# Performance work log

Measured on AMD Instinct MI355X. Metric: run time of the kernel, lower is better.

Reference implementation:

```python
import jax, jax.numpy as jnp
import numpy as np

N_NODES = 50000
N_EDGES = 800000
IN_NF = 128
OUT_NF = 128
HID = 128
EDGE_NF = 16
N_LAYERS = 4
EPS = 1e-5


def _ln(x, g, b):
    mu = jnp.mean(x, axis=-1, keepdims=True)
    var = jnp.mean(jnp.square(x - mu), axis=-1, keepdims=True)
    return (x - mu) * jax.lax.rsqrt(var + EPS) * g + b


def setup_inputs() -> dict:
    key = jax.random.key(0)
    ks = iter(jax.random.split(key, 64))

    def lin(out_d, in_d):
        w = jax.random.normal(next(ks), (out_d, in_d), dtype=jnp.float32) * 0.02
        b = jnp.zeros((out_d,), dtype=jnp.float32)
        return w, b

    def stack(fn):
        outs = [fn() for _ in range(N_LAYERS)]
        return tuple(jnp.stack([o[i] for o in outs]) for i in range(len(outs[0])))

    h = jax.random.normal(next(ks), (N_NODES, IN_NF), dtype=jnp.float32)
    edges = jax.random.randint(next(ks), (2, N_EDGES), 0, N_NODES, dtype=jnp.int32)
    edge_attr = jax.random.normal(next(ks), (N_EDGES, EDGE_NF), dtype=jnp.float32)

    emb_in_w1, emb_in_b1 = lin(HID, IN_NF)
    emb_in_w2, emb_in_b2 = lin(HID, HID)
    emb_out_w1, emb_out_b1 = lin(HID, HID)
    emb_out_w2, emb_out_b2 = lin(OUT_NF, HID)

    norm_g, norm_b = stack(lambda: (jnp.ones((HID,), jnp.float32), jnp.zeros((HID,), jnp.float32)))
    edge_w1, edge_b1 = stack(lambda: lin(HID, 2 * HID + EDGE_NF))
    edge_ln_g, edge_ln_b = stack(lambda: (jnp.ones((HID,), jnp.float32), jnp.zeros((HID,), jnp.float32)))
    edge_w2, edge_b2 = stack(lambda: lin(HID, HID))
    node_w1, node_b1 = stack(lambda: lin(HID, 2 * HID))
    node_ln_g, node_ln_b = stack(lambda: (jnp.ones((HID,), jnp.float32), jnp.zeros((HID,), jnp.float32)))
    node_w2, node_b2 = stack(lambda: lin(HID, HID))

    return dict(h=h, edges=edges, edge_attr=edge_attr,
                emb_in_w1=emb_in_w1, emb_in_b1=emb_in_b1, emb_in_w2=emb_in_w2, emb_in_b2=emb_in_b2,
                norm_g=norm_g, norm_b=norm_b,
                edge_w1=edge_w1, edge_b1=edge_b1, edge_ln_g=edge_ln_g, edge_ln_b=edge_ln_b,
                edge_w2=edge_w2, edge_b2=edge_b2,
                node_w1=node_w1, node_b1=node_b1, node_ln_g=node_ln_g, node_ln_b=node_ln_b,
                node_w2=node_w2, node_b2=node_b2,
                emb_out_w1=emb_out_w1, emb_out_b1=emb_out_b1, emb_out_w2=emb_out_w2, emb_out_b2=emb_out_b2)


def _gnn(h, edges, edge_attr,
         emb_in_w1, emb_in_b1, emb_in_w2, emb_in_b2,
         norm_g, norm_b, edge_w1, edge_b1, edge_ln_g, edge_ln_b, edge_w2, edge_b2,
         node_w1, node_b1, node_ln_g, node_ln_b, node_w2, node_b2,
         emb_out_w1, emb_out_b1, emb_out_w2, emb_out_b2):
    row, col = edges[0], edges[1]
    n = h.shape[0]

    # embedding_in: Linear -> SiLU -> Linear
    h = jax.nn.silu(h @ emb_in_w1.T + emb_in_b1) @ emb_in_w2.T + emb_in_b2

    def layer(h, p):
        (ng, nb, ew1, eb1, elg, elb, ew2, eb2, nw1, nb1, nlg, nlb, nw2, nb2) = p
        hn = _ln(h, ng, nb)                                   # pre-layer LayerNorm
        # message: gather -> Linear -> LN -> SiLU -> Linear
        eh = jnp.concatenate([hn[row], hn[col], edge_attr], axis=1)  # [E, 2H+Ef]
        m = jax.nn.silu(_ln(eh @ ew1.T + eb1, elg, elb)) @ ew2.T + eb2  # [E, H]
        # aggregate: scatter-add over source nodes
        agg = jax.ops.segment_sum(m, row, num_segments=n)     # [N, H]
        cat = jnp.concatenate([hn, agg], axis=1)              # [N, 2H]
        dh = jax.nn.silu(_ln(cat @ nw1.T + nb1, nlg, nlb)) @ nw2.T + nb2
        return hn + dh, None

    params = (norm_g, norm_b, edge_w1, edge_b1, edge_ln_g, edge_ln_b, edge_w2, edge_b2,
              node_w1, node_b1, node_ln_g, node_ln_b, node_w2, node_b2)
    h, _ = jax.lax.scan(layer, h, params)

    # embedding_out
    return jax.nn.silu(h @ emb_out_w1.T + emb_out_b1) @ emb_out_w2.T + emb_out_b2


def reference(h, edges, edge_attr,
              emb_in_w1, emb_in_b1, emb_in_w2, emb_in_b2,
              norm_g, norm_b, edge_w1, edge_b1, edge_ln_g, edge_ln_b, edge_w2, edge_b2,
              node_w1, node_b1, node_ln_g, node_ln_b, node_w2, node_b2,
              emb_out_w1, emb_out_b1, emb_out_w2, emb_out_b2):
    return _gnn(h, edges, edge_attr,
                emb_in_w1, emb_in_b1, emb_in_w2, emb_in_b2,
                norm_g, norm_b, edge_w1, edge_b1, edge_ln_g, edge_ln_b, edge_w2, edge_b2,
                node_w1, node_b1, node_ln_g, node_ln_b, node_w2, node_b2,
                emb_out_w1, emb_out_b1, emb_out_w2, emb_out_b2)
```

## Files before the change

### kernel.cpp

```cpp
#include <hip/hip_runtime.h>
#include <math.h>

#define NN 50000
#define NE 800000
#define HID 128
#define NNH ((size_t)NN * HID)
#define NPAD 50176

typedef __attribute__((ext_vector_type(8))) short short8;
typedef __attribute__((ext_vector_type(4))) float f32x4;
typedef __attribute__((ext_vector_type(2))) _Float16 half2v;
typedef __attribute__((ext_vector_type(8))) _Float16 half8;

__device__ __forceinline__ ushort f2bf(float f) {
  unsigned u = __float_as_uint(f);
  unsigned r = (u + 0x7fffu + ((u >> 16) & 1u)) >> 16;
  return (ushort)r;
}
__device__ __forceinline__ ushort f2h_bits(float f) {
  _Float16 h = (_Float16)f;
  ushort u;
  __builtin_memcpy(&u, &h, 2);
  return u;
}
__device__ __forceinline__ half2v u2h(uint u) {
  half2v h;
  __builtin_memcpy(&h, &u, 4);
  return h;
}
__device__ __forceinline__ float silu_f(float x) { return x / (1.0f + __expf(-x)); }

__device__ __forceinline__ float wsum64(float x) {
  int t;
  t = __builtin_amdgcn_update_dpp(0, __float_as_int(x), 0x111, 0xf, 0xf, true); x += __int_as_float(t);
  t = __builtin_amdgcn_update_dpp(0, __float_as_int(x), 0x112, 0xf, 0xf, true); x += __int_as_float(t);
  t = __builtin_amdgcn_update_dpp(0, __float_as_int(x), 0x114, 0xf, 0xf, true); x += __int_as_float(t);
  t = __builtin_amdgcn_update_dpp(0, __float_as_int(x), 0x118, 0xf, 0xf, true); x += __int_as_float(t);
  t = __builtin_amdgcn_update_dpp(0, __float_as_int(x), 0x142, 0xf, 0xf, true); x += __int_as_float(t);
  t = __builtin_amdgcn_update_dpp(0, __float_as_int(x), 0x143, 0xf, 0xf, true); x += __int_as_float(t);
  return __uint_as_float(__builtin_amdgcn_readlane(__float_as_int(x), 63));
}

__global__ __launch_bounds__(256) void zero_i(int* __restrict__ p, int n)
{
  int i = blockIdx.x * 256 + threadIdx.x;
  if (i < n) p[i] = 0;
}

__global__ __launch_bounds__(256) void count_src(const int* __restrict__ src, int* __restrict__ cnt)
{
  int e = blockIdx.x * 256 + threadIdx.x;
  if (e < NE) atomicAdd(&cnt[src[e]], 1);
}

__global__ __launch_bounds__(1024) void scan_excl(const int* __restrict__ cnt, int* __restrict__ base, int n)
{
  __shared__ int ws[16];
  int t = threadIdx.x;
  const int per = (n + 1023) / 1024;
  int s0 = t * per;
  int sum = 0;
  for (int i = 0; i < per; ++i) { int idx = s0 + i; if (idx < n) sum += cnt[idx]; }
  int lane = t & 63, w = t >> 6;
  int v = sum;
  #pragma unroll
  for (int m = 1; m < 64; m <<= 1) { int o = __shfl_up(v, m, 64); if (lane >= m) v += o; }
  if (lane == 63) ws[w] = v;
  __syncthreads();
  if (t == 0) { int a = 0; for (int i = 0; i < 16; ++i) { int x = ws[i]; ws[i] = a; a += x; } }
  __syncthreads();
  int run = ws[w] + v - sum;
  for (int i = 0; i < per; ++i) {
    int idx = s0 + i;
    if (idx < n) { base[idx] = run; run += cnt[idx]; }
  }
}

__global__ __launch_bounds__(256) void place_edges(const int* __restrict__ src, const int* __restrict__ dst,
    const int* __restrict__ base, int* __restrict__ cur,
    int* __restrict__ dst_s, int* __restrict__ perm)
{
  int e = blockIdx.x * 256 + threadIdx.x;
  if (e >= NE) return;
  int s = src[e];
  int p = base[s] + atomicAdd(&cur[s], 1);
  dst_s[p] = dst[e]; perm[p] = e;
}

__global__ __launch_bounds__(256) void permute_ea_h(const float4* __restrict__ ea,
    const int* __restrict__ perm, ushort* __restrict__ ea_s)
{
  int i = blockIdx.x * 256 + threadIdx.x;
  if (i >= NE * 4) return;
  int e = i >> 2, q = i & 3;
  float4 v = ea[(size_t)perm[e] * 4 + q];
  uint2 p;
  p.x = (uint)f2h_bits(v.x) | ((uint)f2h_bits(v.y) << 16);
  p.y = (uint)f2h_bits(v.z) | ((uint)f2h_bits(v.w) << 16);
  *(uint2*)&ea_s[(size_t)e * 16 + q * 4] = p;
}

__global__ __launch_bounds__(256) void cvt4(const float* __restrict__ s0, const float* __restrict__ s1,
    const float* __restrict__ s2, const float* __restrict__ s3, ushort* __restrict__ d)
{
  int i = blockIdx.x * 256 + threadIdx.x;
  if (i >= 65536) return;
  const float* s = (i < 16384) ? s0 : (i < 32768) ? s1 : (i < 49152) ? s2 : s3;
  d[i] = f2bf(s[i & 16383]);
}
__global__ __launch_bounds__(256) void cvt_wab(const float* __restrict__ s, ushort* __restrict__ d)
{
  int i = blockIdx.x * 256 + threadIdx.x;
  if (i >= 131072) return;
  int l = i >> 15, rem = i & 32767;
  int r = rem >> 7, c = rem & 127;
  int srow = r & 127, scol = ((r >> 7) << 7) + c;
  d[l * 104448 + r * 128 + c] = f2bf(s[(size_t)l * 34816 + srow * 272 + scol]);
}
__global__ __launch_bounds__(256) void cvt_std(const float* __restrict__ s, ushort* __restrict__ d,
    int rows, int cols, int lss)
{
  int i = blockIdx.x * 256 + threadIdx.x;
  int n = 4 * rows * cols;
  if (i >= n) return;
  int rc = rows * cols;
  int l = i / rc, rem = i - l * rc;
  d[l * 104448 + rem] = f2bf(s[(size_t)l * lss + rem]);
}

__global__ __launch_bounds__(128) void fold_w(const float* __restrict__ nw1,
    const float* __restrict__ ew2, const float* __restrict__ eb2,
    ushort* __restrict__ wu_base, float* __restrict__ nv)
{
  __shared__ float red[2];
  int bid = blockIdx.x;
  int l = bid >> 7, m = bid & 127;
  int j = threadIdx.x;
  const float* n1row = nw1 + (size_t)l * 32768 + (size_t)m * 256;
  const float* n1b = n1row + 128;
  const float* w2 = ew2 + (size_t)l * 16384;
  float s = 0.f;
  for (int k = 0; k < 128; ++k) s = fmaf(n1b[k], w2[k * 128 + j], s);
  ushort* lb = wu_base + (size_t)l * 104448;
  lb[32768 + m * 128 + j] = f2h_bits(s);
  lb[49152 + m * 128 + j] = f2bf(n1row[j]);
  float p = n1b[j] * eb2[l * 128 + j];
  #pragma unroll
  for (int mm = 1; mm < 64; mm <<= 1) p += __shfl_xor(p, mm, 64);
  if ((j & 63) == 0) red[j >> 6] = p;
  __syncthreads();
  if (j == 0) nv[l * 128 + m] = red[0] + red[1];
}

template<int FUSE>
__global__ __launch_bounds__(256) void emb2(
    const float* __restrict__ A,
    const ushort* __restrict__ W1, const float* __restrict__ b1,
    const ushort* __restrict__ W2, const float* __restrict__ b2,
    const float* __restrict__ lg, const float* __restrict__ lbp,
    const ushort* __restrict__ Wab, const float* __restrict__ eb1,
    float* __restrict__ Hn, float* __restrict__ Pa, float* __restrict__ Pb,
    float* __restrict__ C, int n)
{
  __shared__ ushort Al[64][136];
  const int tid = threadIdx.x;
  const int n0 = blockIdx.x * 64;

  #pragma unroll
  for (int i = 0; i < 8; ++i) {
    int s = tid + i * 256;
    int row = s >> 5, c4 = (s & 31) * 4;
    int gr = n0 + row;
    float4 v = make_float4(0.f, 0.f, 0.f, 0.f);
    if (gr < n) v = *(const float4*)(A + (size_t)gr * HID + c4);
    uint2 p;
    p.x = (uint)f2bf(v.x) | ((uint)f2bf(v.y) << 16);
    p.y = (uint)f2bf(v.z) | ((uint)f2bf(v.w) << 16);
    *(uint2*)&Al[row][c4] = p;
  }
  __syncthreads();

  const int w = tid >> 6, l = tid & 63;
  const int lr = l & 15, lh = l >> 4;

  f32x4 zf = {0.f, 0.f, 0.f, 0.f};
  f32x4 acc[8];
  #pragma unroll
  for (int nt = 0; nt < 8; ++nt) acc[nt] = zf;

  #pragma unroll
  for (int q = 0; q < 4; ++q) {
    short8 af = *(const short8*)&Al[w * 16 + lr][q * 32 + lh * 8];
    #pragma unroll
    for (int nt = 0; nt < 8; ++nt) {
      short8 bf = *(const short8*)(W1 + (size_t)(nt * 16 + lr) * HID + q * 32 + lh * 8);
      acc[nt] = __builtin_amdgcn_mfma_f32_16x16x32_bf16(af, bf, acc[nt], 0, 0, 0);
    }
  }

  float vb[8];
  #pragma unroll
  for (int nt = 0; nt < 8; ++nt) vb[nt] = b1[nt * 16 + lr];

  #pragma unroll
  for (int r = 0; r < 4; ++r) {
    int row = w * 16 + lh * 4 + r;
    #pragma unroll
    for (int nt = 0; nt < 8; ++nt)
      Al[row][nt * 16 + lr] = f2bf(silu_f(acc[nt][r] + vb[nt]));
  }

  f32x4 acc2[8];
  #pragma unroll
  for (int nt = 0; nt < 8; ++nt) acc2[nt] = zf;
  #pragma unroll
  for (int q = 0; q < 4; ++q) {
    short8 af = *(const short8*)&Al[w * 16 + lr][q * 32 + lh * 8];
    #pragma unroll
    for (int nt = 0; nt < 8; ++nt) {
      short8 bf = *(const short8*)(W2 + (size_t)(nt * 16 + lr) * HID + q * 32 + lh * 8);
      acc2[nt] = __builtin_amdgcn_mfma_f32_16x16x32_bf16(af, bf, acc2[nt], 0, 0, 0);
    }
  }

  float vb2[8];
  #pragma unroll
  for (int nt = 0; nt < 8; ++nt) vb2[nt] = b2[nt * 16 + lr];

  if (FUSE == 0) {
    #pragma unroll
    for (int r = 0; r < 4; ++r) {
      int row = n0 + w * 16 + lh * 4 + r;
      if (row < n) {
        float* cr = C + (size_t)row * HID;
        #pragma unroll
        for (int nt = 0; nt < 8; ++nt)
          cr[nt * 16 + lr] = acc2[nt][r] + vb2[nt];
      }
    }
    return;
  }

  float gv[8], bv[8];
  #pragma unroll
  for (int nt = 0; nt < 8; ++nt) { gv[nt] = lg[nt * 16 + lr]; bv[nt] = lbp[nt * 16 + lr]; }

  #pragma unroll
  for (int r = 0; r < 4; ++r) {
    int row = n0 + w * 16 + lh * 4 + r;
    bool ok = row < n;
    float vals[8];
    #pragma unroll
    for (int nt = 0; nt < 8; ++nt) vals[nt] = acc2[nt][r] + vb2[nt];
    float s1 = 0.f, s2 = 0.f;
    #pragma unroll
    for (int nt = 0; nt < 8; ++nt) { s1 += vals[nt]; s2 += vals[nt] * vals[nt]; }
    #pragma unroll
    for (int m = 1; m < 16; m <<= 1) { s1 += __shfl_xor(s1, m, 64); s2 += __shfl_xor(s2, m, 64); }
    float mu = s1 * (1.0f / 128.0f);
    float var = s2 * (1.0f / 128.0f) - mu * mu;
    float rs = rsqrtf(var + 1e-5f);
    int lrow = w * 16 + lh * 4 + r;
    float* hnr = Hn + (size_t)row * HID;
    #pragma unroll
    for (int nt = 0; nt < 8; ++nt) {
      float hn = (vals[nt] - mu) * rs * gv[nt] + bv[nt];
      if (ok) hnr[nt * 16 + lr] = hn;
      Al[lrow][nt * 16 + lr] = f2bf(hn);
    }
  }

  f32x4 aab[16];
  #pragma unroll
  for (int nt = 0; nt < 16; ++nt) aab[nt] = zf;
  #pragma unroll
  for (int q = 0; q < 4; ++q) {
    short8 af = *(const short8*)&Al[w * 16 + lr][q * 32 + lh * 8];
    #pragma unroll
    for (int nt = 0; nt < 16; ++nt) {
      short8 bf = *(const short8*)(Wab + (size_t)(nt * 16 + lr) * HID + q * 32 + lh * 8);
      aab[nt] = __builtin_amdgcn_mfma_f32_16x16x32_bf16(af, bf, aab[nt], 0, 0, 0);
    }
  }
  float be[8];
  #pragma unroll
  for (int nt = 0; nt < 8; ++nt) be[nt] = eb1[nt * 16 + lr];
  #pragma unroll
  for (int r = 0; r < 4; ++r) {
    int row = n0 + w * 16 + lh * 4 + r;
    if (row >= n) break;
    float* pa = Pa + (size_t)row * HID;
    float* pb = Pb + (size_t)row * HID;
    #pragma unroll
    for (int nt = 0; nt < 8; ++nt) {
      int col = nt * 16 + lr;
      pa[col] = aab[nt][r] + be[nt];
      pb[col] = aab[nt + 8][r];
    }
  }
}

__global__ __launch_bounds__(256) void node_edge(
    const float* __restrict__ Pa, const float* __restrict__ Pb,
    const ushort* __restrict__ ea_h,
    const int* __restrict__ dst_s,
    const int* __restrict__ ebase, const int* __restrict__ deg,
    const float* __restrict__ w1c,
    const float* __restrict__ elg, const float* __restrict__ elb,
    ushort* __restrict__ Sh, int n)
{
  const int tid = threadIdx.x;
  const int wv = __builtin_amdgcn_readfirstlane(tid >> 6);
  const int lane = tid & 63;
  const int node = blockIdx.x * 4 + wv;
  if (node >= n) return;
  const int c0 = lane * 2;

  half2v w1h0[8], w1h1[8];
  {
    const float* wr0 = w1c + (size_t)c0 * 272 + 256;
    const float* wr1 = wr0 + 272;
    #pragma unroll
    for (int k = 0; k < 8; ++k) {
      half2v h0; h0[0] = (_Float16)wr0[2 * k]; h0[1] = (_Float16)wr0[2 * k + 1]; w1h0[k] = h0;
      half2v h1; h1[0] = (_Float16)wr1[2 * k]; h1[1] = (_Float16)wr1[2 * k + 1]; w1h1[k] = h1;
    }
  }
  const float g0 = elg[c0], g1 = elg[c0 + 1];
  const float b0 = elb[c0], b1 = elb[c0 + 1];
  const float pax = Pa[(size_t)node * HID + c0];
  const float pay = Pa[(size_t)node * HID + c0 + 1];

  const int beg = __builtin_amdgcn_readfirstlane(ebase[node]);
  const int dg  = __builtin_amdgcn_readfirstlane(deg[node]);

  float a0 = 0.f, a1 = 0.f;

  uint4 eA0 = make_uint4(0,0,0,0), eB0 = eA0, eA1 = eA0, eB1 = eA0;
  float2 p0 = make_float2(0.f, 0.f), p1 = p0;

  auto LOADE = [&](int idx, uint4& ea, uint4& eb, float2& pb) {
    int eu = __builtin_amdgcn_readfirstlane(beg + idx);
    int d  = dst_s[eu];
    ea = *(const uint4*)(ea_h + (size_t)eu * 16);
    eb = *(const uint4*)(ea_h + (size_t)eu * 16 + 8);
    pb = *(const float2*)(Pb + (size_t)d * HID + c0);
  };
  auto PROCESS = [&](const uint4& eaA, const uint4& eaB, const float2& pbc) {
    half2v eh[8];
    eh[0] = u2h(eaA.x); eh[1] = u2h(eaA.y); eh[2] = u2h(eaA.z); eh[3] = u2h(eaA.w);
    eh[4] = u2h(eaB.x); eh[5] = u2h(eaB.y); eh[6] = u2h(eaB.z); eh[7] = u2h(eaB.w);

    float x0 = pax + pbc.x;
    float x1 = pay + pbc.y;
    #pragma unroll
    for (int k = 0; k < 8; ++k) {
      x0 = __builtin_amdgcn_fdot2(eh[k], w1h0[k], x0, false);
      x1 = __builtin_amdgcn_fdot2(eh[k], w1h1[k], x1, false);
    }
    float s1 = wsum64(x0 + x1);
    float s2 = wsum64(fmaf(x0, x0, x1 * x1));
    float mu = s1 * (1.0f / 128.0f);
    float var = s2 * (1.0f / 128.0f) - mu * mu;
    float rs = rsqrtf(var + 1e-5f);
    a0 += silu_f((x0 - mu) * rs * g0 + b0);
    a1 += silu_f((x1 - mu) * rs * g1 + b1);
  };

  if (dg > 0) LOADE(0, eA0, eB0, p0);
  if (dg > 1) LOADE(1, eA1, eB1, p1);

  for (int i = 0; i < dg; i += 2) {
    uint4 nA0 = make_uint4(0,0,0,0), nB0 = nA0, nA1 = nA0, nB1 = nA0;
    float2 np0 = make_float2(0.f, 0.f), np1 = np0;
    if (i + 2 < dg) LOADE(i + 2, nA0, nB0, np0);
    if (i + 3 < dg) LOADE(i + 3, nA1, nB1, np1);

    PROCESS(eA0, eB0, p0);
    if (i + 1 < dg) PROCESS(eA1, eB1, p1);

    eA0 = nA0; eB0 = nB0; p0 = np0;
    eA1 = nA1; eB1 = nB1; p1 = np1;
  }

  uint pk = (uint)f2h_bits(a0) | ((uint)f2h_bits(a1) << 16);
  *(uint*)(Sh + (size_t)node * HID + c0) = pk;
}

template<int FUSE>
__global__ __launch_bounds__(256) void node_mlp(
    const float* __restrict__ Hn, const ushort* __restrict__ Sh,
    const ushort* __restrict__ N1a, const ushort* __restrict__ W2Nh, const ushort* __restrict__ N2,
    const float* __restrict__ nb1, const float* __restrict__ nv, const int* __restrict__ deg,
    const float* __restrict__ lng, const float* __restrict__ lnb, const float* __restrict__ nb2,
    const float* __restrict__ lg2, const float* __restrict__ lb2p,
    const ushort* __restrict__ Wab2, const float* __restrict__ eb1_2,
    float* __restrict__ HnOut, float* __restrict__ Pa, float* __restrict__ Pb,
    float* __restrict__ C, int n)
{
  __shared__ ushort Ahn[64][136];
  __shared__ ushort Ash[64][136];
  const int tid = threadIdx.x;
  const int n0 = blockIdx.x * 64;

  #pragma unroll
  for (int i = 0; i < 8; ++i) {
    int s = tid + i * 256;
    int row = s >> 5, c4 = (s & 31) * 4;
    int gr = n0 + row;
    float4 vh = make_float4(0.f, 0.f, 0.f, 0.f);
    uint2 sv = make_uint2(0, 0);
    if (gr < n) {
      vh = *(const float4*)(Hn + (size_t)gr * HID + c4);
      sv = *(const uint2*)(Sh + (size_t)gr * HID + c4);
    }
    uint2 ph;
    ph.x = (uint)f2bf(vh.x) | ((uint)f2bf(vh.y) << 16);
    ph.y = (uint)f2bf(vh.z) | ((uint)f2bf(vh.w) << 16);
    *(uint2*)&Ahn[row][c4] = ph;
    *(uint2*)&Ash[row][c4] = sv;
  }
  __syncthreads();

  const int w = tid >> 6, l = tid & 63;
  const int lr = l & 15, lh = l >> 4;

  f32x4 zf = {0.f, 0.f, 0.f, 0.f};
  f32x4 acc[8];
  #pragma unroll
  for (int nt = 0; nt < 8; ++nt) acc[nt] = zf;

  #pragma unroll
  for (int q = 0; q < 4; ++q) {
    short8 an = *(const short8*)&Ahn[w * 16 + lr][q * 32 + lh * 8];
    half8  as = *(const half8*)&Ash[w * 16 + lr][q * 32 + lh * 8];
    #pragma unroll
    for (int nt = 0; nt < 8; ++nt) {
      short8 b1f = *(const short8*)(N1a + (size_t)(nt * 16 + lr) * HID + q * 32 + lh * 8);
      half8  b2h = *(const half8*)(W2Nh + (size_t)(nt * 16 + lr) * HID + q * 32 + lh * 8);
      acc[nt] = __builtin_amdgcn_mfma_f32_16x16x32_bf16(an, b1f, acc[nt], 0, 0, 0);
      acc[nt] = __builtin_amdgcn_mfma_f32_16x16x32_f16(as, b2h, acc[nt], 0, 0, 0);
    }
  }

  float vb[8], vn[8], gv[8], bv[8];
  #pragma unroll
  for (int nt = 0; nt < 8; ++nt) {
    int col = nt * 16 + lr;
    vb[nt] = nb1[col]; vn[nt] = nv[col];
    gv[nt] = lng[col]; bv[nt] = lnb[col];
  }

  #pragma unroll
  for (int r = 0; r < 4; ++r) {
    int row = n0 + w * 16 + lh * 4 + r;
    float degf = (row < n) ? (float)deg[row] : 0.f;
    float vals[8];
    #pragma unroll
    for (int nt = 0; nt < 8; ++nt) vals[nt] = acc[nt][r] + vb[nt] + degf * vn[nt];
    float s1 = 0.f, s2 = 0.f;
    #pragma unroll
    for (int nt = 0; nt < 8; ++nt) { s1 += vals[nt]; s2 += vals[nt] * vals[nt]; }
    #pragma unroll
    for (int m = 1; m < 16; m <<= 1) { s1 += __shfl_xor(s1, m, 64); s2 += __shfl_xor(s2, m, 64); }
    float mu = s1 * (1.0f / 128.0f);
    float var = s2 * (1.0f / 128.0f) - mu * mu;
    float rs = rsqrtf(var + 1e-5f);
    int lrow = w * 16 + lh * 4 + r;
    #pragma unroll
    for (int nt = 0; nt < 8; ++nt)
      Ahn[lrow][nt * 16 + lr] = f2bf(silu_f((vals[nt] - mu) * rs * gv[nt] + bv[nt]));
  }

  f32x4 acc2[8];
  #pragma unroll
  for (int nt = 0; nt < 8; ++nt) acc2[nt] = zf;
  #pragma unroll
  for (int q = 0; q < 4; ++q) {
    short8 af = *(const short8*)&Ahn[w * 16 + lr][q * 32 + lh * 8];
    #pragma unroll
    for (int nt = 0; nt < 8; ++nt) {
      short8 bf = *(const short8*)(N2 + (size_t)(nt * 16 + lr) * HID + q * 32 + lh * 8);
      acc2[nt] = __builtin_amdgcn_mfma_f32_16x16x32_bf16(af, bf, acc2[nt], 0, 0, 0);
    }
  }

  float vb2[8];
  #pragma unroll
  for (int nt = 0; nt < 8; ++nt) vb2[nt] = nb2[nt * 16 + lr];

  if (FUSE == 0) {
    #pragma unroll
    for (int r = 0; r < 4; ++r) {
      int row = n0 + w * 16 + lh * 4 + r;
      if (row < n) {
        const float* hr = Hn + (size_t)row * HID;
        float* cr = C + (size_t)row * HID;
        #pragma unroll
        for (int nt = 0; nt < 8; ++nt) {
          int col = nt * 16 + lr;
          cr[col] = hr[col] + acc2[nt][r] + vb2[nt];
        }
      }
    }
    return;
  }

  float gv2[8], bv2[8];
  #pragma unroll
  for (int nt = 0; nt < 8; ++nt) { gv2[nt] = lg2[nt * 16 + lr]; bv2[nt] = lb2p[nt * 16 + lr]; }

  #pragma unroll
  for (int r = 0; r < 4; ++r) {
    int row = n0 + w * 16 + lh * 4 + r;
    bool ok = row < n;
    const float* hr = Hn + (size_t)row * HID;
    float vals[8];
    #pragma unroll
    for (int nt = 0; nt < 8; ++nt) {
      int col = nt * 16 + lr;
      float base = ok ? hr[col] : 0.f;
      vals[nt] = base + acc2[nt][r] + vb2[nt];
    }
    float s1 = 0.f, s2 = 0.f;
    #pragma unroll
    for (int nt = 0; nt < 8; ++nt) { s1 += vals[nt]; s2 += vals[nt] * vals[nt]; }
    #pragma unroll
    for (int m = 1; m < 16; m <<= 1) { s1 += __shfl_xor(s1, m, 64); s2 += __shfl_xor(s2, m, 64); }
    float mu = s1 * (1.0f / 128.0f);
    float var = s2 * (1.0f / 128.0f) - mu * mu;
    float rs = rsqrtf(var + 1e-5f);
    int lrow = w * 16 + lh * 4 + r;
    float* hnr = HnOut + (size_t)row * HID;
    #pragma unroll
    for (int nt = 0; nt < 8; ++nt) {
      float hn = (vals[nt] - mu) * rs * gv2[nt] + bv2[nt];
      if (ok) hnr[nt * 16 + lr] = hn;
      Ahn[lrow][nt * 16 + lr] = f2bf(hn);
    }
  }

  f32x4 aab[16];
  #pragma unroll
  for (int nt = 0; nt < 16; ++nt) aab[nt] = zf;
  #pragma unroll
  for (int q = 0; q < 4; ++q) {
    short8 af = *(const short8*)&Ahn[w * 16 + lr][q * 32 + lh * 8];
    #pragma unroll
    for (int nt = 0; nt < 16; ++nt) {
      short8 bf = *(const short8*)(Wab2 + (size_t)(nt * 16 + lr) * HID + q * 32 + lh * 8);
      aab[nt] = __builtin_amdgcn_mfma_f32_16x16x32_bf16(af, bf, aab[nt], 0, 0, 0);
    }
  }
  float be[8];
  #pragma unroll
  for (int nt = 0; nt < 8; ++nt) be[nt] = eb1_2[nt * 16 + lr];
  #pragma unroll
  for (int r = 0; r < 4; ++r) {
    int row = n0 + w * 16 + lh * 4 + r;
    if (row >= n) break;
    float* pa = Pa + (size_t)row * HID;
    float* pb = Pb + (size_t)row * HID;
    #pragma unroll
    for (int nt = 0; nt < 8; ++nt) {
      int col = nt * 16 + lr;
      pa[col] = aab[nt][r] + be[nt];
      pb[col] = aab[nt + 8][r];
    }
  }
}

extern "C" void kernel_launch(void* const* d_in, const int* in_sizes, int n_in,
                              void* d_out, int out_size, void* d_ws, size_t ws_size,
                              hipStream_t stream)
{
  const float* in_h  = (const float*)d_in[0];
  const int*   edges = (const int*)d_in[1];
  const float* ea    = (const float*)d_in[2];
  const float* ei_w1 = (const float*)d_in[3];
  const float* ei_b1 = (const float*)d_in[4];
  const float* ei_w2 = (const float*)d_in[5];
  const float* ei_b2 = (const float*)d_in[6];
  const float* ng    = (const float*)d_in[7];
  const float* nbp   = (const float*)d_in[8];
  const float* ew1   = (const float*)d_in[9];
  const float* eb1   = (const float*)d_in[10];
  const float* elg   = (const float*)d_in[11];
  const float* elb   = (const float*)d_in[12];
  const float* ew2   = (const float*)d_in[13];
  const float* eb2   = (const float*)d_in[14];
  const float* nw1   = (const float*)d_in[15];
  const float* nb1   = (const float*)d_in[16];
  const float* nlg   = (const float*)d_in[17];
  const float* nlb   = (const float*)d_in[18];
  const float* nw2   = (const float*)d_in[19];
  const float* nb2   = (const float*)d_in[20];
  const float* eo_w1 = (const float*)d_in[21];
  const float* eo_b1 = (const float*)d_in[22];
  const float* eo_w2 = (const float*)d_in[23];
  const float* eo_b2 = (const float*)d_in[24];

  float* wf    = (float*)d_ws;
  float* B_h   = wf;
  float* B_hn  = wf + NNH;
  float* B_S   = wf + 2 * NNH;
  float* B_tmp = wf + 3 * NNH;
  float* B_pb  = wf + 4 * NNH;
  ushort* Sh   = (ushort*)B_S;

  const size_t WOFF = 5 * NNH;
  ushort* wu = (ushort*)(wf + WOFF);
  const size_t SOFF = WOFF + 262144;
  int* dst_s = (int*)(wf + SOFF);
  int* cnt   = dst_s + NE;
  int* cur   = cnt + NPAD;
  int* base  = cur + NPAD;
  ushort* ea_s = (ushort*)(base + NPAD);
  float* nvb = (float*)(ea_s + (size_t)NE * 16);
  int* perm  = (int*)B_S;

  const int NB  = (NN + 63) / 64;
  const int NBE = (NN + 3) / 4;
  const int NEB = (NE + 255) / 256;

  const int* erow = edges;
  const int* ecol = edges + NE;

  zero_i<<<(2 * NPAD + 255) / 256, 256, 0, stream>>>(cnt, 2 * NPAD);
  count_src<<<NEB, 256, 0, stream>>>(erow, cnt);
  scan_excl<<<1, 1024, 0, stream>>>(cnt, base, NN);
  place_edges<<<NEB, 256, 0, stream>>>(erow, ecol, base, cur, dst_s, perm);
  permute_ea_h<<<(NE * 4 + 255) / 256, 256, 0, stream>>>((const float4*)ea, perm, ea_s);

  cvt4<<<256, 256, 0, stream>>>(ei_w1, ei_w2, eo_w1, eo_w2, wu);
  cvt_wab<<<512, 256, 0, stream>>>(ew1, wu + 65536);
  cvt_std<<<(4 * 16384 + 255) / 256, 256, 0, stream>>>(nw2, wu + 65536 + 81920, 128, 128, 16384);
  fold_w<<<512, 128, 0, stream>>>(nw1, ew2, eb2, wu + 65536, nvb);

  emb2<1><<<NB, 256, 0, stream>>>(in_h, wu, ei_b1, wu + 16384, ei_b2,
      ng, nbp, wu + 65536, eb1, B_hn, B_tmp, B_pb, nullptr, NN);

  for (int lyr = 0; lyr < 4; ++lyr) {
    ushort* lb = wu + 65536 + lyr * 104448;
    node_edge<<<NBE, 256, 0, stream>>>(B_tmp, B_pb, ea_s, dst_s, base, cnt,
        ew1 + 34816 * lyr, elg + 128 * lyr, elb + 128 * lyr, Sh, NN);
    if (lyr < 3) {
      ushort* lb2 = lb + 104448;
      node_mlp<1><<<NB, 256, 0, stream>>>(B_hn, Sh, lb + 49152, lb + 32768, lb + 81920,
          nb1 + 128 * lyr, nvb + 128 * lyr, cnt,
          nlg + 128 * lyr, nlb + 128 * lyr, nb2 + 128 * lyr,
          ng + 128 * (lyr + 1), nbp + 128 * (lyr + 1), lb2, eb1 + 128 * (lyr + 1),
          B_hn, B_tmp, B_pb, nullptr, NN);
    } else {
      node_mlp<0><<<NB, 256, 0, stream>>>(B_hn, Sh, lb + 49152, lb + 32768, lb + 81920,
          nb1 + 128 * lyr, nvb + 128 * lyr, cnt,
          nlg + 128 * lyr, nlb + 128 * lyr, nb2 + 128 * lyr,
          nullptr, nullptr, nullptr, nullptr,
          nullptr, nullptr, nullptr, B_h, NN);
    }
  }

  emb2<0><<<NB, 256, 0, stream>>>(B_h, wu + 32768, eo_b1, wu + 49152, eo_b2,
      nullptr, nullptr, nullptr, nullptr, nullptr, nullptr, nullptr, (float*)d_out, NN);
}
```

Before: 1.216 ms.

## Store edge projections Pa/Pb in fp16 and fuse edge-attr permutation into placement

```diff
diff --git a/kernel.cpp b/kernel.cpp
--- a/kernel.cpp
+++ b/kernel.cpp
@@ -77,27 +77,29 @@
 }
 
 __global__ __launch_bounds__(256) void place_edges(const int* __restrict__ src, const int* __restrict__ dst,
+    const float4* __restrict__ ea,
     const int* __restrict__ base, int* __restrict__ cur,
-    int* __restrict__ dst_s, int* __restrict__ perm)
+    int* __restrict__ dst_s, ushort* __restrict__ ea_s)
 {
   int e = blockIdx.x * 256 + threadIdx.x;
   if (e >= NE) return;
   int s = src[e];
   int p = base[s] + atomicAdd(&cur[s], 1);
-  dst_s[p] = dst[e]; perm[p] = e;
-}
-
-__global__ __launch_bounds__(256) void permute_ea_h(const float4* __restrict__ ea,
-    const int* __restrict__ perm, ushort* __restrict__ ea_s)
-{
-  int i = blockIdx.x * 256 + threadIdx.x;
-  if (i >= NE * 4) return;
-  int e = i >> 2, q = i & 3;
-  float4 v = ea[(size_t)perm[e] * 4 + q];
-  uint2 p;
-  p.x = (uint)f2h_bits(v.x) | ((uint)f2h_bits(v.y) << 16);
-  p.y = (uint)f2h_bits(v.z) | ((uint)f2h_bits(v.w) << 16);
-  *(uint2*)&ea_s[(size_t)e * 16 + q * 4] = p;
+  dst_s[p] = dst[e];
+  const float4* ef = ea + (size_t)e * 4;
+  float4 v0 = ef[0], v1 = ef[1], v2 = ef[2], v3 = ef[3];
+  uint4 o0, o1;
+  o0.x = (uint)f2h_bits(v0.x) | ((uint)f2h_bits(v0.y) << 16);
+  o0.y = (uint)f2h_bits(v0.z) | ((uint)f2h_bits(v0.w) << 16);
+  o0.z = (uint)f2h_bits(v1.x) | ((uint)f2h_bits(v1.y) << 16);
+  o0.w = (uint)f2h_bits(v1.z) | ((uint)f2h_bits(v1.w) << 16);
+  o1.x = (uint)f2h_bits(v2.x) | ((uint)f2h_bits(v2.y) << 16);
+  o1.y = (uint)f2h_bits(v2.z) | ((uint)f2h_bits(v2.w) << 16);
+  o1.z = (uint)f2h_bits(v3.x) | ((uint)f2h_bits(v3.y) << 16);
+  o1.w = (uint)f2h_bits(v3.z) | ((uint)f2h_bits(v3.w) << 16);
+  ushort* dp = ea_s + (size_t)p * 16;
+  *(uint4*)dp = o0;
+  *(uint4*)(dp + 8) = o1;
 }
 
 __global__ __launch_bounds__(256) void cvt4(const float* __restrict__ s0, const float* __restrict__ s1,
@@ -159,7 +161,7 @@
     const ushort* __restrict__ W2, const float* __restrict__ b2,
     const float* __restrict__ lg, const float* __restrict__ lbp,
     const ushort* __restrict__ Wab, const float* __restrict__ eb1,
-    float* __restrict__ Hn, float* __restrict__ Pa, float* __restrict__ Pb,
+    float* __restrict__ Hn, ushort* __restrict__ Pa, ushort* __restrict__ Pb,
     float* __restrict__ C, int n)
 {
   __shared__ ushort Al[64][136];
@@ -289,19 +291,19 @@
   for (int r = 0; r < 4; ++r) {
     int row = n0 + w * 16 + lh * 4 + r;
     if (row >= n) break;
-    float* pa = Pa + (size_t)row * HID;
-    float* pb = Pb + (size_t)row * HID;
+    ushort* pa = Pa + (size_t)row * HID;
+    ushort* pb = Pb + (size_t)row * HID;
     #pragma unroll
     for (int nt = 0; nt < 8; ++nt) {
       int col = nt * 16 + lr;
-      pa[col] = aab[nt][r] + be[nt];
-      pb[col] = aab[nt + 8][r];
+      pa[col] = f2h_bits(aab[nt][r] + be[nt]);
+      pb[col] = f2h_bits(aab[nt + 8][r]);
     }
   }
 }
 
 __global__ __launch_bounds__(256) void node_edge(
-    const float* __restrict__ Pa, const float* __restrict__ Pb,
+    const ushort* __restrict__ Pah, const ushort* __restrict__ Pbh,
     const ushort* __restrict__ ea_h,
     const int* __restrict__ dst_s,
     const int* __restrict__ ebase, const int* __restrict__ deg,
@@ -328,8 +330,9 @@
   }
   const float g0 = elg[c0], g1 = elg[c0 + 1];
   const float b0 = elb[c0], b1 = elb[c0 + 1];
-  const float pax = Pa[(size_t)node * HID + c0];
-  const float pay = Pa[(size_t)node * HID + c0 + 1];
+  half2v pav = u2h(*(const uint*)(Pah + (size_t)node * HID + c0));
+  const float pax = (float)pav[0];
+  const float pay = (float)pav[1];
 
   const int beg = __builtin_amdgcn_readfirstlane(ebase[node]);
   const int dg  = __builtin_amdgcn_readfirstlane(deg[node]);
@@ -337,22 +340,23 @@
   float a0 = 0.f, a1 = 0.f;
 
   uint4 eA0 = make_uint4(0,0,0,0), eB0 = eA0, eA1 = eA0, eB1 = eA0;
-  float2 p0 = make_float2(0.f, 0.f), p1 = p0;
-
-  auto LOADE = [&](int idx, uint4& ea, uint4& eb, float2& pb) {
+  uint p0 = 0, p1 = 0;
+
+  auto LOADE = [&](int idx, uint4& ea, uint4& eb, uint& pb) {
     int eu = __builtin_amdgcn_readfirstlane(beg + idx);
     int d  = dst_s[eu];
     ea = *(const uint4*)(ea_h + (size_t)eu * 16);
     eb = *(const uint4*)(ea_h + (size_t)eu * 16 + 8);
-    pb = *(const float2*)(Pb + (size_t)d * HID + c0);
+    pb = *(const uint*)(Pbh + (size_t)d * HID + c0);
   };
-  auto PROCESS = [&](const uint4& eaA, const uint4& eaB, const float2& pbc) {
+  auto PROCESS = [&](const uint4& eaA, const uint4& eaB, uint pbu) {
     half2v eh[8];
     eh[0] = u2h(eaA.x); eh[1] = u2h(eaA.y); eh[2] = u2h(eaA.z); eh[3] = u2h(eaA.w);
     eh[4] = u2h(eaB.x); eh[5] = u2h(eaB.y); eh[6] = u2h(eaB.z); eh[7] = u2h(eaB.w);
-
-    float x0 = pax + pbc.x;
-    float x1 = pay + pbc.y;
+    half2v pb2 = u2h(pbu);
+
+    float x0 = pax + (float)pb2[0];
+    float x1 = pay + (float)pb2[1];
     #pragma unroll
     for (int k = 0; k < 8; ++k) {
       x0 = __builtin_amdgcn_fdot2(eh[k], w1h0[k], x0, false);
@@ -372,7 +376,7 @@
 
   for (int i = 0; i < dg; i += 2) {
     uint4 nA0 = make_uint4(0,0,0,0), nB0 = nA0, nA1 = nA0, nB1 = nA0;
-    float2 np0 = make_float2(0.f, 0.f), np1 = np0;
+    uint np0 = 0, np1 = 0;
     if (i + 2 < dg) LOADE(i + 2, nA0, nB0, np0);
     if (i + 3 < dg) LOADE(i + 3, nA1, nB1, np1);
 
@@ -395,7 +399,7 @@
     const float* __restrict__ lng, const float* __restrict__ lnb, const float* __restrict__ nb2,
     const float* __restrict__ lg2, const float* __restrict__ lb2p,
     const ushort* __restrict__ Wab2, const float* __restrict__ eb1_2,
-    float* __restrict__ HnOut, float* __restrict__ Pa, float* __restrict__ Pb,
+    float* __restrict__ HnOut, ushort* __restrict__ Pa, ushort* __restrict__ Pb,
     float* __restrict__ C, int n)
 {
   __shared__ ushort Ahn[64][136];
@@ -559,13 +563,13 @@
   for (int r = 0; r < 4; ++r) {
     int row = n0 + w * 16 + lh * 4 + r;
     if (row >= n) break;
-    float* pa = Pa + (size_t)row * HID;
-    float* pb = Pb + (size_t)row * HID;
+    ushort* pa = Pa + (size_t)row * HID;
+    ushort* pb = Pb + (size_t)row * HID;
     #pragma unroll
     for (int nt = 0; nt < 8; ++nt) {
       int col = nt * 16 + lr;
-      pa[col] = aab[nt][r] + be[nt];
-      pb[col] = aab[nt + 8][r];
+      pa[col] = f2h_bits(aab[nt][r] + be[nt]);
+      pb[col] = f2h_bits(aab[nt + 8][r]);
     }
   }
 }
@@ -607,6 +611,8 @@
   float* B_tmp = wf + 3 * NNH;
   float* B_pb  = wf + 4 * NNH;
   ushort* Sh   = (ushort*)B_S;
+  ushort* Pah  = (ushort*)B_tmp;
+  ushort* Pbh  = (ushort*)B_pb;
 
   const size_t WOFF = 5 * NNH;
   ushort* wu = (ushort*)(wf + WOFF);
@@ -617,7 +623,6 @@
   int* base  = cur + NPAD;
   ushort* ea_s = (ushort*)(base + NPAD);
   float* nvb = (float*)(ea_s + (size_t)NE * 16);
-  int* perm  = (int*)B_S;
 
   const int NB  = (NN + 63) / 64;
   const int NBE = (NN + 3) / 4;
@@ -629,8 +634,7 @@
   zero_i<<<(2 * NPAD + 255) / 256, 256, 0, stream>>>(cnt, 2 * NPAD);
   count_src<<<NEB, 256, 0, stream>>>(erow, cnt);
   scan_excl<<<1, 1024, 0, stream>>>(cnt, base, NN);
-  place_edges<<<NEB, 256, 0, stream>>>(erow, ecol, base, cur, dst_s, perm);
-  permute_ea_h<<<(NE * 4 + 255) / 256, 256, 0, stream>>>((const float4*)ea, perm, ea_s);
+  place_edges<<<NEB, 256, 0, stream>>>(erow, ecol, (const float4*)ea, base, cur, dst_s, ea_s);
 
   cvt4<<<256, 256, 0, stream>>>(ei_w1, ei_w2, eo_w1, eo_w2, wu);
   cvt_wab<<<512, 256, 0, stream>>>(ew1, wu + 65536);
@@ -638,11 +642,11 @@
   fold_w<<<512, 128, 0, stream>>>(nw1, ew2, eb2, wu + 65536, nvb);
 
   emb2<1><<<NB, 256, 0, stream>>>(in_h, wu, ei_b1, wu + 16384, ei_b2,
-      ng, nbp, wu + 65536, eb1, B_hn, B_tmp, B_pb, nullptr, NN);
+      ng, nbp, wu + 65536, eb1, B_hn, Pah, Pbh, nullptr, NN);
 
   for (int lyr = 0; lyr < 4; ++lyr) {
     ushort* lb = wu + 65536 + lyr * 104448;
-    node_edge<<<NBE, 256, 0, stream>>>(B_tmp, B_pb, ea_s, dst_s, base, cnt,
+    node_edge<<<NBE, 256, 0, stream>>>(Pah, Pbh, ea_s, dst_s, base, cnt,
         ew1 + 34816 * lyr, elg + 128 * lyr, elb + 128 * lyr, Sh, NN);
     if (lyr < 3) {
       ushort* lb2 = lb + 104448;
@@ -650,7 +654,7 @@
           nb1 + 128 * lyr, nvb + 128 * lyr, cnt,
           nlg + 128 * lyr, nlb + 128 * lyr, nb2 + 128 * lyr,
           ng + 128 * (lyr + 1), nbp + 128 * (lyr + 1), lb2, eb1 + 128 * (lyr + 1),
-          B_hn, B_tmp, B_pb, nullptr, NN);
+          B_hn, Pah, Pbh, nullptr, NN);
     } else {
       node_mlp<0><<<NB, 256, 0, stream>>>(B_hn, Sh, lb + 49152, lb + 32768, lb + 81920,
           nb1 + 128 * lyr, nvb + 128 * lyr, cnt,
```

Result: faster. 1.165 ms (-4.2%).
